# Kernel optimization log

Measured on AMD Instinct MI355X. Metric: run time of the kernel, lower is better.

The kernel has to match this reference:

```python
import jax, jax.numpy as jnp
import numpy as np

GAMMA = 0.997
LAMDA = 0.95


def setup_inputs() -> dict:
    key = jax.random.key(0)
    k1, k2, k3, k4 = jax.random.split(key, 4)
    B, T = 131072, 64
    return {
        "predicted_continue_logits": jax.random.normal(k1, (B, T), dtype=jnp.float32),
        "rewards": jax.random.normal(k2, (B, T), dtype=jnp.float32),
        "continues": jax.random.uniform(k3, (B, T), dtype=jnp.float32),
        "critic_values": jax.random.normal(k4, (B, T), dtype=jnp.float32),
    }


def _lambda_returns(rewards, continues, values, gamma, lamda):
    # rewards/continues/values: [B, T]. Reverse-time recurrence:
    #   R_t = r_t + gamma * c_t * ((1 - lamda) * v_{t+1} + lamda * R_{t+1}),  R_{T-1} bootstrap = v_{T-1}
    r = jnp.swapaxes(rewards[:, :-1], 0, 1)    # [T-1, B]
    c = jnp.swapaxes(continues[:, :-1], 0, 1)  # [T-1, B]
    vn = jnp.swapaxes(values[:, 1:], 0, 1)     # [T-1, B] (v_{t+1})

    def step(carry, x):
        r_t, c_t, vn_t = x
        ret = r_t + gamma * c_t * ((1.0 - lamda) * vn_t + lamda * carry)
        return ret, ret

    bootstrap = values[:, -1]  # [B]
    _, rets = jax.lax.scan(step, bootstrap, (r, c, vn), reverse=True)
    return jnp.swapaxes(rets, 0, 1)  # [B, T-1]


def reference(predicted_continue_logits, rewards, continues, critic_values):
    # Bernoulli(logits).probs == sigmoid(logits)
    continue_probs = jax.nn.sigmoid(predicted_continue_logits)  # [B, T]
    lambda_returns = _lambda_returns(rewards, continues, critic_values, GAMMA, LAMDA)  # [B, T-1]
    return continue_probs, lambda_returns
```

## Files before the change

### kernel.cpp

```cpp
#include <hip/hip_runtime.h>


constexpr float GAMMA = 0.997f;
constexpr float LAMDA = 0.95f;
constexpr int T = 64;

__global__ __launch_bounds__(256) void fused_k(const float* __restrict__ logits,
                                               const float* __restrict__ rew,
                                               const float* __restrict__ con,
                                               const float* __restrict__ val,
                                               float* __restrict__ out_sig,
                                               float* __restrict__ out_ret,
                                               int B) {
  const int tid = blockIdx.x * blockDim.x + threadIdx.x;
  const int row = tid >> 6;
  const int t   = tid & 63;
  if (row >= B) return;

  const size_t idx = (size_t)row * T + t;

  const float x = logits[idx];
  out_sig[idx] = 1.0f / (1.0f + __expf(-x));

  const float r = rew[idx];
  const float c = con[idx];
  const float v = val[idx];

  const float vnext = __shfl(v, (t < 63) ? t + 1 : 63);

  float A, Bc;
  if (t == 63) {
    A = 1.0f; Bc = 0.0f;
  } else {
    A  = (GAMMA * LAMDA) * c;
    Bc = fmaf((GAMMA * (1.0f - LAMDA)) * c, vnext, r);
  }

#pragma unroll
  for (int d = 1; d < 64; d <<= 1) {
    int src = t + d;
    if (src > 63) src = 63;
    const float Ain = __shfl(A, src);
    const float Bin = __shfl(Bc, src);
    Bc = fmaf(A, Bin, Bc);
    A  = A * Ain;
  }

  const float v63 = __shfl(v, 63);
  const float ret = fmaf(A, v63, Bc);

  if (t < 63) out_ret[(size_t)row * 63 + t] = ret;
}

extern "C" void kernel_launch(void* const* d_in, const int* in_sizes, int n_in,
                              void* d_out, int out_size, void* d_ws, size_t ws_size,
                              hipStream_t stream) {
  const float* logits = (const float*)d_in[0];
  const float* rew    = (const float*)d_in[1];
  const float* con    = (const float*)d_in[2];
  const float* val    = (const float*)d_in[3];
  float* out = (float*)d_out;

  const int BT = in_sizes[0];
  const int B  = BT / T;

  float* out_sig = out;
  float* out_ret = out + (size_t)BT;

  const int blocks = B / 4;
  fused_k<<<blocks, 256, 0, stream>>>(logits, rew, con, val, out_sig, out_ret, B);
}
```

Measured before the change: 171.6 us.

## Process four timesteps per thread with float4 loads and segmented 16-lane scan

Each thread now handles four consecutive timesteps of a row, loaded as float4, and each wavefront covers four rows. The per-thread chunk is composed serially, then a 4-step segmented shuffle scan over 16 lanes replaces the 6-step 64-lane scan, followed by a serial back-substitution. This cuts shuffle count and thread count and widens memory transactions. The cost is more per-thread work, extra scalar loads for v63 and the next chunk's value, and unaligned scalar stores to the 63-wide output rows.

```diff
diff --git a/kernel.cpp b/kernel.cpp
--- a/kernel.cpp
+++ b/kernel.cpp
@@ -12,44 +12,73 @@
                                                float* __restrict__ out_sig,
                                                float* __restrict__ out_ret,
                                                int B) {
-  const int tid = blockIdx.x * blockDim.x + threadIdx.x;
-  const int row = tid >> 6;
-  const int t   = tid & 63;
+  const int gid  = blockIdx.x * blockDim.x + threadIdx.x;
+  const int wid  = gid >> 6;
+  const int lane = gid & 63;
+  const int g    = lane >> 4;
+  const int q    = lane & 15;
+  const int row  = wid * 4 + g;
   if (row >= B) return;
 
-  const size_t idx = (size_t)row * T + t;
+  const size_t rbase = (size_t)row * T;
+  constexpr float GL  = GAMMA * LAMDA;
+  constexpr float G1L = GAMMA * (1.0f - LAMDA);
 
-  const float x = logits[idx];
-  out_sig[idx] = 1.0f / (1.0f + __expf(-x));
+  const float4 x = ((const float4*)(logits + rbase))[q];
+  const float4 r = ((const float4*)(rew    + rbase))[q];
+  const float4 c = ((const float4*)(con    + rbase))[q];
+  const float4 v = ((const float4*)(val    + rbase))[q];
+  const float v63 = val[rbase + 63];
+  const float vnx = val[rbase + ((q < 15) ? 4 * q + 4 : 63)];
 
-  const float r = rew[idx];
-  const float c = con[idx];
-  const float v = val[idx];
+  float4 s;
+  s.x = 1.0f / (1.0f + __expf(-x.x));
+  s.y = 1.0f / (1.0f + __expf(-x.y));
+  s.z = 1.0f / (1.0f + __expf(-x.z));
+  s.w = 1.0f / (1.0f + __expf(-x.w));
+  ((float4*)(out_sig + rbase))[q] = s;
 
-  const float vnext = __shfl(v, (t < 63) ? t + 1 : 63);
+  const float a0 = GL * c.x, b0 = fmaf(G1L * c.x, v.y, r.x);
+  const float a1 = GL * c.y, b1 = fmaf(G1L * c.y, v.z, r.y);
+  const float a2 = GL * c.z, b2 = fmaf(G1L * c.z, v.w, r.z);
+  float a3, b3;
+  if (q == 15) { a3 = 1.0f; b3 = 0.0f; }
+  else         { a3 = GL * c.w; b3 = fmaf(G1L * c.w, vnx, r.w); }
 
-  float A, Bc;
-  if (t == 63) {
-    A = 1.0f; Bc = 0.0f;
-  } else {
-    A  = (GAMMA * LAMDA) * c;
-    Bc = fmaf((GAMMA * (1.0f - LAMDA)) * c, vnext, r);
-  }
+  float A = a3, Bb = b3;
+  A = a2 * A; Bb = fmaf(a2, Bb, b2);
+  A = a1 * A; Bb = fmaf(a1, Bb, b1);
+  A = a0 * A; Bb = fmaf(a0, Bb, b0);
 
 #pragma unroll
-  for (int d = 1; d < 64; d <<= 1) {
-    int src = t + d;
-    if (src > 63) src = 63;
-    const float Ain = __shfl(A, src);
-    const float Bin = __shfl(Bc, src);
-    Bc = fmaf(A, Bin, Bc);
+  for (int d = 1; d < 16; d <<= 1) {
+    int src = lane + d; if (src > 63) src = 63;
+    float Ain = __shfl(A, src);
+    float Bin = __shfl(Bb, src);
+    const bool ok = (q + d) < 16;
+    Ain = ok ? Ain : 1.0f;
+    Bin = ok ? Bin : 0.0f;
+    Bb = fmaf(A, Bin, Bb);
     A  = A * Ain;
   }
 
-  const float v63 = __shfl(v, 63);
-  const float ret = fmaf(A, v63, Bc);
+  int srcx = lane + 1; if (srcx > 63) srcx = 63;
+  float Aex = __shfl(A, srcx);
+  float Bex = __shfl(Bb, srcx);
+  const bool okx = q < 15;
+  Aex = okx ? Aex : 1.0f;
+  Bex = okx ? Bex : 0.0f;
+  const float carry = fmaf(Aex, v63, Bex);
 
-  if (t < 63) out_ret[(size_t)row * 63 + t] = ret;
+  const float c3 = fmaf(a3, carry, b3);
+  const float c2 = fmaf(a2, c3, b2);
+  const float c1 = fmaf(a1, c2, b1);
+  const float c0 = fmaf(a0, c1, b0);
+  float* orow = out_ret + (size_t)row * 63 + 4 * q;
+  orow[0] = c0;
+  orow[1] = c1;
+  orow[2] = c2;
+  if (q < 15) orow[3] = c3;
 }
 
 extern "C" void kernel_launch(void* const* d_in, const int* in_sizes, int n_in,
@@ -67,6 +96,6 @@
   float* out_sig = out;
   float* out_ret = out + (size_t)BT;
 
-  const int blocks = B / 4;
+  const int blocks = (B + 15) / 16;
   fused_k<<<blocks, 256, 0, stream>>>(logits, rew, con, val, out_sig, out_ret, B);
 }
```

New measurement: 175.1 us. 1.02x slower.
